# Performance work log

Measured on AMD Instinct MI355X. Metric: run time of the kernel, lower is better.

## Reference

```python
import jax, jax.numpy as jnp
import numpy as np

K = 3        # neighbors per point (includes self at distance 0, as in knn_points(x, x))
WEIGHT = 1.0


def setup_inputs() -> dict:
    key = jax.random.key(0)
    k0, k1, k2, k3, k4 = jax.random.split(key, 5)
    B, N = 2, 8192
    return {
        "xyz": jax.random.normal(k0, (B, N, 3), dtype=jnp.float32),
        "rotations": jax.random.normal(k1, (B, N, 4), dtype=jnp.float32),
        "scales": jax.random.normal(k2, (B, N, 3), dtype=jnp.float32),
        "colors": jax.random.normal(k3, (B, N, 45), dtype=jnp.float32),
        "opacity": jax.random.normal(k4, (B, N, 1), dtype=jnp.float32),
    }


def _knn(xyz, k):
    # Brute-force self-KNN: squared euclidean distances, k smallest (sorted ascending).
    sq = jnp.sum(xyz * xyz, axis=-1)                       # [N]
    d = sq[:, None] + sq[None, :] - 2.0 * (xyz @ xyz.T)    # [N, N] squared distances
    neg_d, idx = jax.lax.top_k(-d, k)                      # k nearest -> largest of -d
    return -neg_d, idx                                     # dist_sq [N,K], nn_ind [N,K]


def _sample_loss(xyz, rot, sc, col, op):
    dist_sq, nn_ind = _knn(xyz, K)
    # gather [N,K,C] per attribute, unbiased std over the K neighbors (torch default ddof=1)
    std_mean = lambda a: jnp.std(a[nn_ind], axis=1, ddof=1).mean()
    return (std_mean(rot) + std_mean(sc) + std_mean(op) + std_mean(col)
            + dist_sq.mean())


def reference(xyz, rotations, scales, colors, opacity):
    losses = jax.vmap(_sample_loss)(xyz, rotations, scales, colors, opacity)  # [B]
    return jnp.sum(losses) / xyz.shape[0] * WEIGHT
```

## Files before the change

kernel.cpp:

```cpp
#include <hip/hip_runtime.h>
#include <stdint.h>

#define NPTS 8192
#define CTILE 1024
#define NTILES (NPTS / CTILE)
#define BLK 512
#define QPB 32
#define BLKS_PER_BATCH (NPTS / QPB)

typedef __attribute__((ext_vector_type(8)))  short short8;
typedef __attribute__((ext_vector_type(16))) float float16;

__device__ __forceinline__ uint32_t umin32(uint32_t a, uint32_t b) { return a < b ? a : b; }
__device__ __forceinline__ uint32_t umax32(uint32_t a, uint32_t b) { return a > b ? a : b; }

__device__ __forceinline__ void ins3(uint32_t key, uint32_t& k0, uint32_t& k1, uint32_t& k2) {
    uint32_t a = umin32(k0, key);
    uint32_t b = umax32(k0, key);
    k0 = a;
    uint32_t c = umin32(k1, b);
    uint32_t d = umax32(k1, b);
    k1 = c;
    k2 = umin32(k2, d);
}

__device__ __forceinline__ uint16_t f2bf(float x) {
    uint32_t u = __float_as_uint(x);
    return (uint16_t)((u + 0x7FFFu + ((u >> 16) & 1u)) >> 16);
}
__device__ __forceinline__ float bf2f(uint16_t s) {
    return __uint_as_float((uint32_t)s << 16);
}

__global__ __launch_bounds__(256) void pack_kernel(
    const float* __restrict__ xyz, uint4* __restrict__ ws, int total)
{
    int t = blockIdx.x * 256 + threadIdx.x;
    if (t >= total) return;
    int b = t >> 13;
    int n = t & (NPTS - 1);
    const float* p = xyz + ((size_t)b * NPTS + n) * 3;
    float cx = p[0], cy = p[1], cz = p[2];
    uint16_t bhx = f2bf(cx), bhy = f2bf(cy), bhz = f2bf(cz);
    uint16_t blx = f2bf(cx - bf2f(bhx));
    uint16_t bly = f2bf(cy - bf2f(bhy));
    uint16_t blz = f2bf(cz - bf2f(bhz));
    float nc = fmaf(cz, cz, fmaf(cy, cy, cx * cx));
    uint16_t nch = f2bf(nc), ncl = f2bf(nc - bf2f(nch));
    const uint32_t ONE = 0x3F80u;
    uint4 a0, a1;
    a0.x = (uint32_t)bhx | ((uint32_t)bhy << 16);
    a0.y = (uint32_t)bhz | ((uint32_t)blx << 16);
    a0.z = (uint32_t)bly | ((uint32_t)blz << 16);
    a0.w = ONE | (ONE << 16);
    a1.x = (uint32_t)bhx | ((uint32_t)bhy << 16);
    a1.y = (uint32_t)bhz | ((uint32_t)nch << 16);
    a1.z = (uint32_t)ncl;
    a1.w = 0u;
    size_t base = (size_t)b * (2 * NPTS);
    ws[base + n]        = a0;
    ws[base + NPTS + n] = a1;
}

__device__ __forceinline__ float point_contrib(
    int j0, int j1, int j2,
    int lane, float xp, float yp, float zp,
    const float* __restrict__ xb,
    const float* __restrict__ rot, const float* __restrict__ sc,
    const float* __restrict__ col, const float* __restrict__ opac,
    size_t abase, float inv_nb)
{
    int c = lane;
    const float* basep = nullptr;
    int stridec = 0, ch = 0;
    float w = 0.0f;
    if (c < 4)       { basep = rot  + abase * 4;  stridec = 4;  ch = c;     w = inv_nb * (1.0f / 4.0f); }
    else if (c < 7)  { basep = sc   + abase * 3;  stridec = 3;  ch = c - 4; w = inv_nb * (1.0f / 3.0f); }
    else if (c == 7) { basep = opac + abase;      stridec = 1;  ch = 0;     w = inv_nb; }
    else if (c < 53) { basep = col  + abase * 45; stridec = 45; ch = c - 8; w = inv_nb * (1.0f / 45.0f); }

    if (basep != nullptr) {
        float v0 = basep[(size_t)j0 * stridec + ch];
        float v1 = basep[(size_t)j1 * stridec + ch];
        float v2 = basep[(size_t)j2 * stridec + ch];
        float mn = (v0 + v1 + v2) * (1.0f / 3.0f);
        float e0 = v0 - mn, e1 = v1 - mn, e2 = v2 - mn;
        return w * sqrtf((e0 * e0 + e1 * e1 + e2 * e2) * 0.5f);
    }
    if (c == 53) {
        float dx = xb[j0 * 3 + 0] - xp, dy = xb[j0 * 3 + 1] - yp, dz = xb[j0 * 3 + 2] - zp;
        float ds = fmaf(dz, dz, fmaf(dy, dy, dx * dx));
        dx = xb[j1 * 3 + 0] - xp; dy = xb[j1 * 3 + 1] - yp; dz = xb[j1 * 3 + 2] - zp;
        ds += fmaf(dz, dz, fmaf(dy, dy, dx * dx));
        dx = xb[j2 * 3 + 0] - xp; dy = xb[j2 * 3 + 1] - yp; dz = xb[j2 * 3 + 2] - zp;
        ds += fmaf(dz, dz, fmaf(dy, dy, dx * dx));
        return ds * (inv_nb * (1.0f / 3.0f));
    }
    return 0.0f;
}

__global__ __launch_bounds__(BLK) void knn_mfma_kernel(
    const float* __restrict__ xyz,
    const float* __restrict__ rot,
    const float* __restrict__ sc,
    const float* __restrict__ colr,
    const float* __restrict__ opac,
    const uint4* __restrict__ pk,
    float* __restrict__ out,
    float inv_nb)
{
    __shared__ __align__(16) uint4 sbuf4[2 * CTILE];
    __shared__ int top3j[QPB * 3];
    __shared__ float blockAcc;
    uint32_t* sbufw = (uint32_t*)sbuf4;

    const int tid  = threadIdx.x;
    const int lane = tid & 63;
    const int wv   = tid >> 6;
    const int qcol = lane & 31;
    const int hl   = lane >> 5;
    const int bb   = blockIdx.x / BLKS_PER_BATCH;
    const int qbase = (blockIdx.x % BLKS_PER_BATCH) * QPB;
    const float* xb = xyz + (size_t)bb * NPTS * 3;
    const uint4* pkb = pk + (size_t)bb * (2 * NPTS);

    if (tid == 0) blockAcc = 0.0f;

    const int qm = qbase + qcol;
    const float qx = xb[qm * 3 + 0], qy = xb[qm * 3 + 1], qz = xb[qm * 3 + 2];
    const float ax = -2.0f * qx, ay = -2.0f * qy, az = -2.0f * qz;
    const uint16_t ahx = f2bf(ax), ahy = f2bf(ay), ahz = f2bf(az);
    const uint16_t alx = f2bf(ax - bf2f(ahx));
    const uint16_t aly = f2bf(ay - bf2f(ahy));
    const uint16_t alz = f2bf(az - bf2f(ahz));
    const float nqe = fmaf(qz, qz, fmaf(qy, qy, qx * qx)) + 1e-3f;
    const uint16_t nqh = f2bf(nqe), nql = f2bf(nqe - bf2f(nqh));
    short8 A;
    if (hl == 0) {
        A[0] = (short)ahx; A[1] = (short)ahy; A[2] = (short)ahz;
        A[3] = (short)ahx; A[4] = (short)ahy; A[5] = (short)ahz;
        A[6] = (short)nqh; A[7] = (short)nql;
    } else {
        A[0] = (short)alx; A[1] = (short)aly; A[2] = (short)alz;
        A[3] = (short)0x3F80; A[4] = (short)0x3F80;
        A[5] = 0; A[6] = 0; A[7] = 0;
    }
    const float16 Z = (float16)0.0f;

    uint32_t k0 = ~0u, k1 = ~0u, k2 = ~0u, k3 = ~0u, k4 = ~0u, k5 = ~0u, k6 = ~0u, k7 = ~0u;
    uint32_t k8 = ~0u, k9 = ~0u, k10 = ~0u, k11 = ~0u, k12 = ~0u, k13 = ~0u, k14 = ~0u, k15 = ~0u;

    const int boff = hl * (CTILE * 16) + (wv * 128 + qcol) * 16;

    for (int T = 0; T < NTILES; ++T) {
        __syncthreads();
#pragma unroll
        for (int s = 0; s < 4; ++s) {
            int slot = s * BLK + tid;
            int n = (slot & (CTILE - 1)) + T * CTILE;
            sbuf4[slot] = pkb[(slot >> 10) * NPTS + n];
        }
        __syncthreads();

        const uint32_t nb0 = (uint32_t)(T * CTILE + wv * 128) + (uint32_t)qcol;
#pragma unroll
        for (int t = 0; t < 4; ++t) {
            short8 Bf = *(const short8*)((const char*)sbuf4 + boff + t * 512);
            float16 D = __builtin_amdgcn_mfma_f32_32x32x16_bf16(A, Bf, Z, 0, 0, 0);
            const uint32_t jj = nb0 + (uint32_t)(t * 32);
#define KU(i, ki) ki = umin32(ki, (__float_as_uint(D[i]) & 0xFFFFE000u) | jj)
            KU(0, k0);  KU(1, k1);  KU(2, k2);  KU(3, k3);
            KU(4, k4);  KU(5, k5);  KU(6, k6);  KU(7, k7);
            KU(8, k8);  KU(9, k9);  KU(10, k10); KU(11, k11);
            KU(12, k12); KU(13, k13); KU(14, k14); KU(15, k15);
#undef KU
        }
    }

    __syncthreads();
    {
        const int base = hl * 1024 + wv * 32 + qcol;
        sbufw[base +    0] = k0;   sbufw[base +  256] = k1;
        sbufw[base +  512] = k2;   sbufw[base +  768] = k3;
        sbufw[base + 2048] = k4;   sbufw[base + 2304] = k5;
        sbufw[base + 2560] = k6;   sbufw[base + 2816] = k7;
        sbufw[base + 4096] = k8;   sbufw[base + 4352] = k9;
        sbufw[base + 4608] = k10;  sbufw[base + 4864] = k11;
        sbufw[base + 6144] = k12;  sbufw[base + 6400] = k13;
        sbufw[base + 6656] = k14;  sbufw[base + 6912] = k15;
    }
    __syncthreads();

    {
        const int g = lane >> 4, li = lane & 15;
        const int row = wv * 4 + g;
        uint32_t K0 = ~0u, K1 = ~0u, K2 = ~0u;
#pragma unroll
        for (int s = 0; s < 16; ++s) ins3(sbufw[row * 256 + li + s * 16], K0, K1, K2);
#pragma unroll
        for (int mk = 1; mk < 16; mk <<= 1) {
            uint32_t r0 = (uint32_t)__shfl_xor((int)K0, mk);
            uint32_t r1 = (uint32_t)__shfl_xor((int)K1, mk);
            uint32_t r2 = (uint32_t)__shfl_xor((int)K2, mk);
            ins3(r0, K0, K1, K2);
            ins3(r1, K0, K1, K2);
            ins3(r2, K0, K1, K2);
        }
        if (li == 0) {
            top3j[row * 3 + 0] = (int)(K0 & 8191u);
            top3j[row * 3 + 1] = (int)(K1 & 8191u);
            top3j[row * 3 + 2] = (int)(K2 & 8191u);
        }
    }
    __syncthreads();

    float acc = 0.0f;
    const size_t abase = (size_t)bb * NPTS;
    for (int i = 0; i < 4; ++i) {
        const int q = wv * 4 + i;
        const int j0 = top3j[q * 3 + 0];
        const int j1 = top3j[q * 3 + 1];
        const int j2 = top3j[q * 3 + 2];
        const int qi = qbase + q;
        const float xp = xb[qi * 3 + 0], yp = xb[qi * 3 + 1], zp = xb[qi * 3 + 2];
        acc += point_contrib(j0, j1, j2, lane, xp, yp, zp,
                             xb, rot, sc, colr, opac, abase, inv_nb);
    }

#pragma unroll
    for (int off = 32; off > 0; off >>= 1) acc += __shfl_xor(acc, off);
    if (lane == 0) atomicAdd(&blockAcc, acc);
    __syncthreads();
    if (tid == 0) atomicAdd(out, blockAcc);
}

extern "C" void kernel_launch(void* const* d_in, const int* in_sizes, int n_in,
                              void* d_out, int out_size, void* d_ws, size_t ws_size,
                              hipStream_t stream) {
    const float* xyz  = (const float*)d_in[0];
    const float* rot  = (const float*)d_in[1];
    const float* sc   = (const float*)d_in[2];
    const float* colr = (const float*)d_in[3];
    const float* opac = (const float*)d_in[4];
    float* out = (float*)d_out;

    const int B = in_sizes[0] / (NPTS * 3);
    const float inv_nb = 1.0f / ((float)NPTS * (float)B);
    const int total = B * NPTS;

    hipMemsetAsync(out, 0, sizeof(float), stream);
    pack_kernel<<<dim3((total + 255) / 256), dim3(256), 0, stream>>>(
        xyz, (uint4*)d_ws, total);
    knn_mfma_kernel<<<dim3(B * BLKS_PER_BATCH), dim3(BLK), 0, stream>>>(
        xyz, rot, sc, colr, opac, (const uint4*)d_ws, out, inv_nb);
}
```

Measured before the change: 93.03 us.

## Fuse bf16 split packing into KNN kernel and double candidate tile size

Removes the separate pack kernel and its workspace round-trip. Each block now reads raw xyz and builds the hi/lo bf16 operands and norms directly into shared memory. The candidate tile grows from 1024 to 2048 points, halving the tile loop count and its barriers, and the inner MFMA loop is partially unrolled. This saves a kernel launch and global traffic, but every block redoes the packing arithmetic for all 8192 points and uses twice the LDS, which may reduce occupancy.

After: 87.24 us. 1.07x faster.

```diff
diff --git a/kernel.cpp b/kernel.cpp
--- a/kernel.cpp
+++ b/kernel.cpp
@@ -2,7 +2,7 @@
 #include <stdint.h>
 
 #define NPTS 8192
-#define CTILE 1024
+#define CTILE 2048
 #define NTILES (NPTS / CTILE)
 #define BLK 512
 #define QPB 32
@@ -30,36 +30,6 @@
 }
 __device__ __forceinline__ float bf2f(uint16_t s) {
     return __uint_as_float((uint32_t)s << 16);
-}
-
-__global__ __launch_bounds__(256) void pack_kernel(
-    const float* __restrict__ xyz, uint4* __restrict__ ws, int total)
-{
-    int t = blockIdx.x * 256 + threadIdx.x;
-    if (t >= total) return;
-    int b = t >> 13;
-    int n = t & (NPTS - 1);
-    const float* p = xyz + ((size_t)b * NPTS + n) * 3;
-    float cx = p[0], cy = p[1], cz = p[2];
-    uint16_t bhx = f2bf(cx), bhy = f2bf(cy), bhz = f2bf(cz);
-    uint16_t blx = f2bf(cx - bf2f(bhx));
-    uint16_t bly = f2bf(cy - bf2f(bhy));
-    uint16_t blz = f2bf(cz - bf2f(bhz));
-    float nc = fmaf(cz, cz, fmaf(cy, cy, cx * cx));
-    uint16_t nch = f2bf(nc), ncl = f2bf(nc - bf2f(nch));
-    const uint32_t ONE = 0x3F80u;
-    uint4 a0, a1;
-    a0.x = (uint32_t)bhx | ((uint32_t)bhy << 16);
-    a0.y = (uint32_t)bhz | ((uint32_t)blx << 16);
-    a0.z = (uint32_t)bly | ((uint32_t)blz << 16);
-    a0.w = ONE | (ONE << 16);
-    a1.x = (uint32_t)bhx | ((uint32_t)bhy << 16);
-    a1.y = (uint32_t)bhz | ((uint32_t)nch << 16);
-    a1.z = (uint32_t)ncl;
-    a1.w = 0u;
-    size_t base = (size_t)b * (2 * NPTS);
-    ws[base + n]        = a0;
-    ws[base + NPTS + n] = a1;
 }
 
 __device__ __forceinline__ float point_contrib(
@@ -105,7 +75,6 @@
     const float* __restrict__ sc,
     const float* __restrict__ colr,
     const float* __restrict__ opac,
-    const uint4* __restrict__ pk,
     float* __restrict__ out,
     float inv_nb)
 {
@@ -122,7 +91,6 @@
     const int bb   = blockIdx.x / BLKS_PER_BATCH;
     const int qbase = (blockIdx.x % BLKS_PER_BATCH) * QPB;
     const float* xb = xyz + (size_t)bb * NPTS * 3;
-    const uint4* pkb = pk + (size_t)bb * (2 * NPTS);
 
     if (tid == 0) blockAcc = 0.0f;
 
@@ -150,21 +118,38 @@
     uint32_t k0 = ~0u, k1 = ~0u, k2 = ~0u, k3 = ~0u, k4 = ~0u, k5 = ~0u, k6 = ~0u, k7 = ~0u;
     uint32_t k8 = ~0u, k9 = ~0u, k10 = ~0u, k11 = ~0u, k12 = ~0u, k13 = ~0u, k14 = ~0u, k15 = ~0u;
 
-    const int boff = hl * (CTILE * 16) + (wv * 128 + qcol) * 16;
+    const int boff = (hl * CTILE + wv * 256 + qcol) * 16;
 
     for (int T = 0; T < NTILES; ++T) {
         __syncthreads();
 #pragma unroll
-        for (int s = 0; s < 4; ++s) {
-            int slot = s * BLK + tid;
-            int n = (slot & (CTILE - 1)) + T * CTILE;
-            sbuf4[slot] = pkb[(slot >> 10) * NPTS + n];
+        for (int s = 0; s < CTILE / BLK; ++s) {
+            int nl = s * BLK + tid;
+            const float* p = xb + (size_t)(T * CTILE + nl) * 3;
+            float cx = p[0], cy = p[1], cz = p[2];
+            uint16_t bhx = f2bf(cx), bhy = f2bf(cy), bhz = f2bf(cz);
+            uint16_t blx = f2bf(cx - bf2f(bhx));
+            uint16_t bly = f2bf(cy - bf2f(bhy));
+            uint16_t blz = f2bf(cz - bf2f(bhz));
+            float nc = fmaf(cz, cz, fmaf(cy, cy, cx * cx));
+            uint16_t nch = f2bf(nc), ncl = f2bf(nc - bf2f(nch));
+            uint4 a0, a1;
+            a0.x = (uint32_t)bhx | ((uint32_t)bhy << 16);
+            a0.y = (uint32_t)bhz | ((uint32_t)blx << 16);
+            a0.z = (uint32_t)bly | ((uint32_t)blz << 16);
+            a0.w = 0x3F80u | (0x3F80u << 16);
+            a1.x = (uint32_t)bhx | ((uint32_t)bhy << 16);
+            a1.y = (uint32_t)bhz | ((uint32_t)nch << 16);
+            a1.z = (uint32_t)ncl;
+            a1.w = 0u;
+            sbuf4[nl]         = a0;
+            sbuf4[CTILE + nl] = a1;
         }
         __syncthreads();
 
-        const uint32_t nb0 = (uint32_t)(T * CTILE + wv * 128) + (uint32_t)qcol;
-#pragma unroll
-        for (int t = 0; t < 4; ++t) {
+        const uint32_t nb0 = (uint32_t)(T * CTILE + wv * 256) + (uint32_t)qcol;
+#pragma unroll 2
+        for (int t = 0; t < 8; ++t) {
             short8 Bf = *(const short8*)((const char*)sbuf4 + boff + t * 512);
             float16 D = __builtin_amdgcn_mfma_f32_32x32x16_bf16(A, Bf, Z, 0, 0, 0);
             const uint32_t jj = nb0 + (uint32_t)(t * 32);
@@ -246,11 +231,8 @@
 
     const int B = in_sizes[0] / (NPTS * 3);
     const float inv_nb = 1.0f / ((float)NPTS * (float)B);
-    const int total = B * NPTS;
 
     hipMemsetAsync(out, 0, sizeof(float), stream);
-    pack_kernel<<<dim3((total + 255) / 256), dim3(256), 0, stream>>>(
-        xyz, (uint4*)d_ws, total);
     knn_mfma_kernel<<<dim3(B * BLKS_PER_BATCH), dim3(BLK), 0, stream>>>(
-        xyz, rot, sc, colr, opac, (const uint4*)d_ws, out, inv_nb);
-}
+        xyz, rot, sc, colr, opac, out, inv_nb);
+}
```

## Stream candidate points directly from global memory and fold output zeroing into pack kernel

Applied to the files above, without the earlier changes.

The cooperative LDS tiling of packed candidate points, with its two barriers per tile, is replaced by each lane loading its B-fragment directly from global memory (L2/L1-cached) in a contiguous 1024-point range per wave. LDS now holds only the key buffer for the top-3 reduction. The separate memset of the output is removed and done by thread 0 of the pack kernel instead. The change drops the tile barriers and most LDS traffic, at the cost of depending on cache hit rates and per-wave global load latency.

Result: faster. 84.74 us, median of 2 (-8.9%).

```diff
diff --git a/kernel.cpp b/kernel.cpp
--- a/kernel.cpp
+++ b/kernel.cpp
@@ -2,8 +2,6 @@
 #include <stdint.h>
 
 #define NPTS 8192
-#define CTILE 1024
-#define NTILES (NPTS / CTILE)
 #define BLK 512
 #define QPB 32
 #define BLKS_PER_BATCH (NPTS / QPB)
@@ -33,9 +31,11 @@
 }
 
 __global__ __launch_bounds__(256) void pack_kernel(
-    const float* __restrict__ xyz, uint4* __restrict__ ws, int total)
+    const float* __restrict__ xyz, uint4* __restrict__ ws,
+    float* __restrict__ out, int total)
 {
     int t = blockIdx.x * 256 + threadIdx.x;
+    if (t == 0) *out = 0.0f;
     if (t >= total) return;
     int b = t >> 13;
     int n = t & (NPTS - 1);
@@ -109,10 +109,9 @@
     float* __restrict__ out,
     float inv_nb)
 {
-    __shared__ __align__(16) uint4 sbuf4[2 * CTILE];
+    __shared__ uint32_t keybuf[QPB * 256];
     __shared__ int top3j[QPB * 3];
     __shared__ float blockAcc;
-    uint32_t* sbufw = (uint32_t*)sbuf4;
 
     const int tid  = threadIdx.x;
     const int lane = tid & 63;
@@ -150,44 +149,37 @@
     uint32_t k0 = ~0u, k1 = ~0u, k2 = ~0u, k3 = ~0u, k4 = ~0u, k5 = ~0u, k6 = ~0u, k7 = ~0u;
     uint32_t k8 = ~0u, k9 = ~0u, k10 = ~0u, k11 = ~0u, k12 = ~0u, k13 = ~0u, k14 = ~0u, k15 = ~0u;
 
-    const int boff = hl * (CTILE * 16) + (wv * 128 + qcol) * 16;
-
-    for (int T = 0; T < NTILES; ++T) {
-        __syncthreads();
-#pragma unroll
-        for (int s = 0; s < 4; ++s) {
-            int slot = s * BLK + tid;
-            int n = (slot & (CTILE - 1)) + T * CTILE;
-            sbuf4[slot] = pkb[(slot >> 10) * NPTS + n];
-        }
-        __syncthreads();
-
-        const uint32_t nb0 = (uint32_t)(T * CTILE + wv * 128) + (uint32_t)qcol;
-#pragma unroll
-        for (int t = 0; t < 4; ++t) {
-            short8 Bf = *(const short8*)((const char*)sbuf4 + boff + t * 512);
-            float16 D = __builtin_amdgcn_mfma_f32_32x32x16_bf16(A, Bf, Z, 0, 0, 0);
-            const uint32_t jj = nb0 + (uint32_t)(t * 32);
+    const int nstart = wv * 1024;
+    const uint4* lanep = pkb + (size_t)hl * NPTS + nstart + qcol;
+    const uint32_t nb0 = (uint32_t)(nstart + qcol);
+#pragma unroll 4
+    for (int t = 0; t < 32; ++t) {
+        uint4 wrd = lanep[t * 32];
+        short8 Bf;
+        Bf[0] = (short)(wrd.x & 0xFFFFu); Bf[1] = (short)(wrd.x >> 16);
+        Bf[2] = (short)(wrd.y & 0xFFFFu); Bf[3] = (short)(wrd.y >> 16);
+        Bf[4] = (short)(wrd.z & 0xFFFFu); Bf[5] = (short)(wrd.z >> 16);
+        Bf[6] = (short)(wrd.w & 0xFFFFu); Bf[7] = (short)(wrd.w >> 16);
+        float16 D = __builtin_amdgcn_mfma_f32_32x32x16_bf16(A, Bf, Z, 0, 0, 0);
+        const uint32_t jj = nb0 + (uint32_t)(t * 32);
 #define KU(i, ki) ki = umin32(ki, (__float_as_uint(D[i]) & 0xFFFFE000u) | jj)
-            KU(0, k0);  KU(1, k1);  KU(2, k2);  KU(3, k3);
-            KU(4, k4);  KU(5, k5);  KU(6, k6);  KU(7, k7);
-            KU(8, k8);  KU(9, k9);  KU(10, k10); KU(11, k11);
-            KU(12, k12); KU(13, k13); KU(14, k14); KU(15, k15);
+        KU(0, k0);  KU(1, k1);  KU(2, k2);  KU(3, k3);
+        KU(4, k4);  KU(5, k5);  KU(6, k6);  KU(7, k7);
+        KU(8, k8);  KU(9, k9);  KU(10, k10); KU(11, k11);
+        KU(12, k12); KU(13, k13); KU(14, k14); KU(15, k15);
 #undef KU
-        }
-    }
-
-    __syncthreads();
+    }
+
     {
         const int base = hl * 1024 + wv * 32 + qcol;
-        sbufw[base +    0] = k0;   sbufw[base +  256] = k1;
-        sbufw[base +  512] = k2;   sbufw[base +  768] = k3;
-        sbufw[base + 2048] = k4;   sbufw[base + 2304] = k5;
-        sbufw[base + 2560] = k6;   sbufw[base + 2816] = k7;
-        sbufw[base + 4096] = k8;   sbufw[base + 4352] = k9;
-        sbufw[base + 4608] = k10;  sbufw[base + 4864] = k11;
-        sbufw[base + 6144] = k12;  sbufw[base + 6400] = k13;
-        sbufw[base + 6656] = k14;  sbufw[base + 6912] = k15;
+        keybuf[base +    0] = k0;   keybuf[base +  256] = k1;
+        keybuf[base +  512] = k2;   keybuf[base +  768] = k3;
+        keybuf[base + 2048] = k4;   keybuf[base + 2304] = k5;
+        keybuf[base + 2560] = k6;   keybuf[base + 2816] = k7;
+        keybuf[base + 4096] = k8;   keybuf[base + 4352] = k9;
+        keybuf[base + 4608] = k10;  keybuf[base + 4864] = k11;
+        keybuf[base + 6144] = k12;  keybuf[base + 6400] = k13;
+        keybuf[base + 6656] = k14;  keybuf[base + 6912] = k15;
     }
     __syncthreads();
 
@@ -196,7 +188,7 @@
         const int row = wv * 4 + g;
         uint32_t K0 = ~0u, K1 = ~0u, K2 = ~0u;
 #pragma unroll
-        for (int s = 0; s < 16; ++s) ins3(sbufw[row * 256 + li + s * 16], K0, K1, K2);
+        for (int s = 0; s < 16; ++s) ins3(keybuf[row * 256 + li + s * 16], K0, K1, K2);
 #pragma unroll
         for (int mk = 1; mk < 16; mk <<= 1) {
             uint32_t r0 = (uint32_t)__shfl_xor((int)K0, mk);
@@ -248,9 +240,8 @@
     const float inv_nb = 1.0f / ((float)NPTS * (float)B);
     const int total = B * NPTS;
 
-    hipMemsetAsync(out, 0, sizeof(float), stream);
     pack_kernel<<<dim3((total + 255) / 256), dim3(256), 0, stream>>>(
-        xyz, (uint4*)d_ws, total);
+        xyz, (uint4*)d_ws, out, total);
     knn_mfma_kernel<<<dim3(B * BLKS_PER_BATCH), dim3(BLK), 0, stream>>>(
         xyz, rot, sc, colr, opac, (const uint4*)d_ws, out, inv_nb);
 }
```
